# Kernel tuning notes

Hardware: AMD Instinct MI355X
Metric: run time of the kernel (lower is better)

The kernel has to match this reference:

```python
import jax, jax.numpy as jnp
import numpy as np

C = 256
GROUPS = 32
EPS = 1e-5

def setup_inputs() -> dict:
    key = jax.random.key(0)
    ks = jax.random.split(key, 7)
    B, H, W = 4, 64, 64
    x = jax.random.normal(ks[0], (B, C, H, W), dtype=jnp.float32)
    # GroupNorm affine params
    gn_w = jnp.ones((C,), dtype=jnp.float32)
    gn_b = jnp.zeros((C,), dtype=jnp.float32)
    # 1x1 conv weights stored as [out, in]
    s = 1.0 / np.sqrt(C)
    qkv_w = jax.random.uniform(ks[1], (3 * C, C), minval=-s, maxval=s, dtype=jnp.float32)
    qkv_b = jax.random.uniform(ks[2], (3 * C,), minval=-s, maxval=s, dtype=jnp.float32)
    proj_w = jax.random.uniform(ks[3], (C, C), minval=-s, maxval=s, dtype=jnp.float32)
    proj_b = jax.random.uniform(ks[4], (C,), minval=-s, maxval=s, dtype=jnp.float32)
    return {"x": x, "gn_w": gn_w, "gn_b": gn_b, "qkv_w": qkv_w,
            "qkv_b": qkv_b, "proj_w": proj_w, "proj_b": proj_b}

def group_norm(x, w, b):
    B, Cc, H, W = x.shape
    xg = x.reshape(B, GROUPS, Cc // GROUPS, H, W)
    mu = xg.mean(axis=(2, 3, 4), keepdims=True)
    var = xg.var(axis=(2, 3, 4), keepdims=True)
    xn = ((xg - mu) * jax.lax.rsqrt(var + EPS)).reshape(B, Cc, H, W)
    return xn * w[None, :, None, None] + b[None, :, None, None]

def reference(x, gn_w, gn_b, qkv_w, qkv_b, proj_w, proj_b):
    B, Cc, H, W = x.shape
    h = group_norm(x, gn_w, gn_b)
    # 1x1 conv == per-pixel matmul
    qkv = jnp.einsum('bchw,oc->bohw', h, qkv_w) + qkv_b[None, :, None, None]
    q, k, v = jnp.split(qkv, 3, axis=1)            # each [B, C, H, W]
    N = H * W
    q = q.reshape(B, Cc, N).transpose(0, 2, 1)      # [B, N, C]
    k = k.reshape(B, Cc, N)                         # [B, C, N]
    v = v.reshape(B, Cc, N).transpose(0, 2, 1)      # [B, N, C]
    w_att = jnp.einsum('bnc,bcm->bnm', q, k) * (Cc ** -0.5)
    w_att = jax.nn.softmax(w_att, axis=-1)
    h = jnp.einsum('bnm,bmc->bnc', w_att, v)        # [B, N, C]
    h = h.transpose(0, 2, 1).reshape(B, Cc, H, W)
    h = jnp.einsum('bchw,oc->bohw', h, proj_w) + proj_b[None, :, None, None]
    return x + h
```

## Files before the change

kernel.cpp:

```cpp
#include <hip/hip_runtime.h>
#include <stdint.h>

typedef unsigned short u16;
typedef __attribute__((ext_vector_type(8))) short bf16x8;
typedef __attribute__((ext_vector_type(4))) float f32x4;

#define BATCH   4
#define CH      256
#define NPIX    4096
#define NGROUPS 32
#define CPG     8
#define EPS     1e-5f

#define NSPLIT 4
#define SPLEN  (NPIX / NSPLIT)
#define ATK    32
#define NIT    (SPLEN / ATK)
#define WSTR   264
#define QTILES 2

__device__ __forceinline__ float bf2f(u16 u) {
    union { uint32_t i; float f; } v; v.i = ((uint32_t)u) << 16; return v.f;
}
__device__ __forceinline__ u16 f2bf(float f) {
    union { float f; uint32_t i; } v; v.f = f;
    uint32_t x = v.i;
    uint32_t r = (x + 0x7fffu + ((x >> 16) & 1u)) >> 16;
    return (u16)r;
}
__device__ __forceinline__ void unpack2(uint32_t u, float& a, float& b) {
    union { uint32_t i; float f; } lo, hi;
    lo.i = u << 16; hi.i = u & 0xffff0000u;
    a = lo.f; b = hi.f;
}
__device__ __forceinline__ void unpack8(uint4 u, float* f) {
    unpack2(u.x, f[0], f[1]); unpack2(u.y, f[2], f[3]);
    unpack2(u.z, f[4], f[5]); unpack2(u.w, f[6], f[7]);
}

__device__ __forceinline__ bool detect_f32(const void* xv) {
    const u16* p = (const u16*)xv;
    int bad = 0;
    #pragma unroll
    for (int i = 0; i < 32; i++) {
        u16 v = p[2 * i];
        int e = (v >> 7) & 0xff;
        bad += (e < 0x68 || e > 0x90) ? 1 : 0;
    }
    return bad >= 10;
}
__device__ __forceinline__ float load1(const void* b, size_t i, bool f32) {
    return f32 ? ((const float*)b)[i] : bf2f(((const u16*)b)[i]);
}
__device__ __forceinline__ void store1(void* b, size_t i, bool f32, float v) {
    if (f32) ((float*)b)[i] = v; else ((u16*)b)[i] = f2bf(v);
}
__device__ __forceinline__ void load4v(const void* base, size_t off, bool f32, float* f) {
    if (f32) {
        float4 a = *(const float4*)((const float*)base + off);
        f[0] = a.x; f[1] = a.y; f[2] = a.z; f[3] = a.w;
    } else {
        uint2 u = *(const uint2*)((const u16*)base + off);
        unpack2(u.x, f[0], f[1]); unpack2(u.y, f[2], f[3]);
    }
}
__device__ __forceinline__ void load8v(const void* base, size_t off, bool f32, float* f) {
    if (f32) {
        const float4* p = (const float4*)((const float*)base + off);
        float4 a = p[0], b = p[1];
        f[0] = a.x; f[1] = a.y; f[2] = a.z; f[3] = a.w;
        f[4] = b.x; f[5] = b.y; f[6] = b.z; f[7] = b.w;
    } else {
        uint4 u = *(const uint4*)((const u16*)base + off);
        unpack8(u, f);
    }
}

__global__ __launch_bounds__(256) void wconv(const void* __restrict__ qkv_w,
                                             const void* __restrict__ proj_w,
                                             u16* __restrict__ wq, u16* __restrict__ wp) {
    bool f32q = detect_f32(qkv_w);
    bool f32p = detect_f32(proj_w);
    int i = blockIdx.x * 256 + threadIdx.x;
    for (int e = i; e < 768 * 256; e += 256 * 256)
        wq[e] = f2bf(load1(qkv_w, e, f32q));
    for (int e = i; e < 256 * 256; e += 256 * 256)
        wp[e] = f2bf(load1(proj_w, e, f32p));
}

__global__ __launch_bounds__(256) void gn_stats(const void* __restrict__ x,
                                                float* __restrict__ stats, int b0) {
    bool f32 = detect_f32(x);
    int bg = b0 * NGROUPS + blockIdx.x;
    int t  = threadIdx.x;
    size_t base = (size_t)bg * (CPG * NPIX);
    float s = 0.f, s2 = 0.f;
    for (int i = t * 8; i < CPG * NPIX; i += 256 * 8) {
        float f[8]; load8v(x, base + i, f32, f);
        #pragma unroll
        for (int e = 0; e < 8; e++) { s += f[e]; s2 += f[e] * f[e]; }
    }
    #pragma unroll
    for (int off = 1; off < 64; off <<= 1) {
        s  += __shfl_xor(s,  off);
        s2 += __shfl_xor(s2, off);
    }
    __shared__ float red[8];
    int w = t >> 6;
    if ((t & 63) == 0) { red[w * 2] = s; red[w * 2 + 1] = s2; }
    __syncthreads();
    if (t == 0) {
        float S  = red[0] + red[2] + red[4] + red[6];
        float S2 = red[1] + red[3] + red[5] + red[7];
        float n  = (float)(CPG * NPIX);
        float mu = S / n;
        float var = S2 / n - mu * mu;
        stats[bg * 2]     = mu;
        stats[bg * 2 + 1] = rsqrtf(var + EPS);
    }
}

__global__ __launch_bounds__(256) void xgn(const void* __restrict__ x,
                                           const void* __restrict__ gn_w,
                                           const void* __restrict__ gn_b,
                                           const float* __restrict__ stats,
                                           u16* __restrict__ xt, int b0) {
    bool f32 = detect_f32(x);
    __shared__ u16 T[64][72];
    int bl = blockIdx.z, bg = b0 + bl;
    int n0 = blockIdx.x * 64, c0 = blockIdx.y * 64;
    int t = threadIdx.x;
    int tc = t >> 4, tn = (t & 15) * 4;
    #pragma unroll
    for (int i = 0; i < 4; i++) {
        int cl = tc + i * 16;
        int c = c0 + cl;
        int g = c >> 3;
        float mu = stats[(bg * NGROUPS + g) * 2];
        float rs = stats[(bg * NGROUPS + g) * 2 + 1];
        float wv = load1(gn_w, c, f32) * rs;
        float bv = load1(gn_b, c, f32) - mu * wv;
        float a[4];
        load4v(x, ((size_t)(bg * CH + c)) * NPIX + n0 + tn, f32, a);
        #pragma unroll
        for (int j = 0; j < 4; j++) T[cl][tn + j] = f2bf(a[j] * wv + bv);
    }
    __syncthreads();
    #pragma unroll
    for (int i = 0; i < 2; i++) {
        int e = t + i * 256;
        int nl = e >> 3, cc = (e & 7) * 8;
        union { uint4 v; u16 s[8]; } pk;
        #pragma unroll
        for (int j = 0; j < 8; j++) pk.s[j] = T[cc + j][nl];
        *(uint4*)(xt + ((size_t)(bl * NPIX) + n0 + nl) * CH + c0 + cc) = pk.v;
    }
}

__global__ __launch_bounds__(256, 3) void qkv_mfma(const u16* __restrict__ xt,
                                                   const u16* __restrict__ wq,
                                                   const void* __restrict__ qkv_b,
                                                   u16* __restrict__ qk,
                                                   u16* __restrict__ vt) {
    __shared__ u16 Ws[64 * WSTR];
    __shared__ u16 T2b[128 * 72];
    bool f32b = detect_f32(qkv_b);
    int bl = blockIdx.z;
    int o0 = blockIdx.y * 64;
    int t = threadIdx.x;
    int w = t >> 6, lane = t & 63;
    int l15 = lane & 15, quad = lane >> 4;

    #pragma unroll
    for (int i = 0; i < 8; i++) {
        int e = t + i * 256;
        *(uint4*)(Ws + (e >> 5) * WSTR + (e & 31) * 8) =
            *(const uint4*)(wq + (size_t)(o0 + (e >> 5)) * CH + (e & 31) * 8);
    }
    __syncthreads();

    bool isv = (o0 >= 512);
    for (int tt = 0; tt < QTILES; tt++) {
        int n0 = (blockIdx.x * QTILES + tt) * 128;
        int pbase = n0 + w * 32;
        const u16* xa = xt + ((size_t)(bl * NPIX + pbase)) * CH;

        f32x4 acc[2][4];
        #pragma unroll
        for (int m = 0; m < 2; m++)
            #pragma unroll
            for (int n = 0; n < 4; n++)
                #pragma unroll
                for (int r = 0; r < 4; r++) acc[m][n][r] = 0.f;

        #pragma unroll
        for (int kc = 0; kc < 8; kc++) {
            bf16x8 a0 = *(const bf16x8*)(xa + (size_t)(l15) * CH + kc * 32 + quad * 8);
            bf16x8 a1 = *(const bf16x8*)(xa + (size_t)(16 + l15) * CH + kc * 32 + quad * 8);
            #pragma unroll
            for (int n = 0; n < 4; n++) {
                bf16x8 b = *(const bf16x8*)(Ws + (n * 16 + l15) * WSTR + kc * 32 + quad * 8);
                acc[0][n] = __builtin_amdgcn_mfma_f32_16x16x32_bf16(a0, b, acc[0][n], 0, 0, 0);
                acc[1][n] = __builtin_amdgcn_mfma_f32_16x16x32_bf16(a1, b, acc[1][n], 0, 0, 0);
            }
        }

        if (!isv) {
            __syncthreads();
            #pragma unroll
            for (int n = 0; n < 4; n++) {
                int o = o0 + n * 16 + l15;
                float bias = load1(qkv_b, o, f32b);
                #pragma unroll
                for (int m = 0; m < 2; m++)
                    #pragma unroll
                    for (int r = 0; r < 4; r++) {
                        int prow = w * 32 + m * 16 + quad * 4 + r;
                        T2b[prow * 72 + n * 16 + l15] = f2bf(acc[m][n][r] + bias);
                    }
            }
            __syncthreads();
            #pragma unroll
            for (int i = 0; i < 4; i++) {
                int e = t + i * 256;
                int p = e >> 3, c = (e & 7) * 8;
                uint4 v = *(const uint4*)(T2b + p * 72 + c);
                *(uint4*)(qk + ((size_t)(bl * NPIX + n0 + p)) * 512 + o0 + c) = v;
            }
        } else {
            #pragma unroll
            for (int n = 0; n < 4; n++) {
                int o = o0 + n * 16 + l15;
                float bias = load1(qkv_b, o, f32b);
                size_t rowb = ((size_t)(bl * CH + o - 512)) * NPIX + pbase;
                #pragma unroll
                for (int m = 0; m < 2; m++) {
                    union { uint2 v; u16 s[4]; } pk;
                    #pragma unroll
                    for (int r = 0; r < 4; r++) pk.s[r] = f2bf(acc[m][n][r] + bias);
                    *(uint2*)(vt + rowb + quad * 8 + m * 4) = pk.v;
                }
            }
        }
    }
}

__global__ __launch_bounds__(256, 2) void attn_mfma(const u16* __restrict__ qk,
                                                    const u16* __restrict__ vt,
                                                    u16* __restrict__ Opart,
                                                    float* __restrict__ lpart,
                                                    int NE, int NR) {
    __shared__ u16 Ks[ATK * 256];
    __shared__ u16 Vts[CH * 32];
    int bl    = blockIdx.z;
    int split = blockIdx.y;
    int q0    = blockIdx.x * 128;
    int t     = threadIdx.x;
    int w     = t >> 6, lane = t & 63;
    int l15   = lane & 15, quad = lane >> 4;

    const u16* qkb = qk + (size_t)bl * NPIX * 512;
    const u16* vtb = vt + (size_t)bl * CH * NPIX;
    int kvbase = split * SPLEN;

    bf16x8 qf[2][8];
    #pragma unroll
    for (int m = 0; m < 2; m++) {
        const u16* qrow = qkb + (size_t)(q0 + w * 32 + m * 16 + l15) * 512;
        #pragma unroll
        for (int kc = 0; kc < 8; kc++)
            qf[m][kc] = *(const bf16x8*)(qrow + kc * 32 + quad * 8);
    }
    f32x4 o[2][16];
    #pragma unroll
    for (int m = 0; m < 2; m++)
        #pragma unroll
        for (int i = 0; i < 16; i++)
            #pragma unroll
            for (int r = 0; r < 4; r++) o[m][i][r] = 0.f;
    float lsum[2] = {0.f, 0.f};
    const float scale = 0.0625f;
    int swz = l15 & 7;

    for (int it = 0; it < NIT; it++) {
        int kv0 = kvbase + it * ATK;
        __syncthreads();
        #pragma unroll
        for (int i = 0; i < 4; i++) {
            int g = t + i * 256;
            int row = g >> 5, pcol = g & 31;
            int lcol = pcol ^ (row & 7);
            __builtin_amdgcn_global_load_lds(
                (const void*)(qkb + (size_t)(kv0 + row) * 512 + 256 + lcol * 8),
                (void*)(Ks + (size_t)g * 8), 16, 0, 0);
        }
        #pragma unroll
        for (int i = 0; i < 4; i++) {
            int g = t + i * 256;
            __builtin_amdgcn_global_load_lds(
                (const void*)(vtb + (size_t)(g >> 2) * NPIX + kv0 + (g & 3) * 8),
                (void*)(Vts + (size_t)g * 8), 16, 0, 0);
        }
        __syncthreads();

        f32x4 sT[2][2];
        #pragma unroll
        for (int kt = 0; kt < 2; kt++)
            #pragma unroll
            for (int qt = 0; qt < 2; qt++)
                #pragma unroll
                for (int r = 0; r < 4; r++) sT[kt][qt][r] = 0.f;
        #pragma unroll
        for (int kc = 0; kc < 8; kc++) {
            int sc = (kc * 4 + quad) ^ swz;
            bf16x8 a0 = *(const bf16x8*)(Ks + l15 * 256 + sc * 8);
            bf16x8 a1 = *(const bf16x8*)(Ks + (16 + l15) * 256 + sc * 8);
            sT[0][0] = __builtin_amdgcn_mfma_f32_16x16x32_bf16(a0, qf[0][kc], sT[0][0], 0, 0, 0);
            sT[0][1] = __builtin_amdgcn_mfma_f32_16x16x32_bf16(a0, qf[1][kc], sT[0][1], 0, 0, 0);
            sT[1][0] = __builtin_amdgcn_mfma_f32_16x16x32_bf16(a1, qf[0][kc], sT[1][0], 0, 0, 0);
            sT[1][1] = __builtin_amdgcn_mfma_f32_16x16x32_bf16(a1, qf[1][kc], sT[1][1], 0, 0, 0);
        }

        bf16x8 pa[2];
        #pragma unroll
        for (int qt = 0; qt < 2; qt++) {
            union { bf16x8 v; u16 s[8]; } pk;
            float ls = 0.f;
            #pragma unroll
            for (int kt = 0; kt < 2; kt++)
                #pragma unroll
                for (int r = 0; r < 4; r++) {
                    float p = __expf(sT[kt][qt][r] * scale);
                    ls += p;
                    pk.s[kt * 4 + r] = f2bf(p);
                }
            lsum[qt] += ls;
            pa[qt] = pk.v;
        }

        #pragma unroll
        for (int dt = 0; dt < 16; dt++) {
            bf16x8 vf = *(const bf16x8*)(Vts + (dt * 16 + l15) * 32 + quad * 8);
            o[0][dt] = __builtin_amdgcn_mfma_f32_16x16x32_bf16(pa[0], vf, o[0][dt], 0, 0, 0);
            o[1][dt] = __builtin_amdgcn_mfma_f32_16x16x32_bf16(pa[1], vf, o[1][dt], 0, 0, 0);
        }
    }

    size_t rowb = (size_t)bl * NPIX + q0 + w * 32;
    u16* op = Opart + (size_t)split * NE;
    #pragma unroll
    for (int qt = 0; qt < 2; qt++) {
        float v = lsum[qt];
        v += __shfl_xor(v, 16); v += __shfl_xor(v, 32);
        if (quad == 0)
            lpart[(size_t)split * NR + rowb + qt * 16 + l15] = v;
        #pragma unroll
        for (int dt = 0; dt < 16; dt++)
            #pragma unroll
            for (int r = 0; r < 4; r++)
                op[(rowb + qt * 16 + quad * 4 + r) * CH + dt * 16 + l15] = f2bf(o[qt][dt][r]);
    }
}

__global__ __launch_bounds__(256, 4) void proj_mfma(const u16* __restrict__ Opart,
                                                    const float* __restrict__ lpart,
                                                    const u16* __restrict__ wp,
                                                    const void* __restrict__ proj_b,
                                                    const void* __restrict__ x,
                                                    void* __restrict__ out,
                                                    int b0, int NE, int NR) {
    __shared__ u16 Ws[64 * WSTR];
    bool f32 = detect_f32(x);
    int bl = blockIdx.z, bg = b0 + bl;
    int n0 = blockIdx.x * 128, o0 = blockIdx.y * 64;
    int t = threadIdx.x;
    int w = t >> 6, lane = t & 63;
    int l15 = lane & 15, quad = lane >> 4;
    int pbase = n0 + w * 32;

    #pragma unroll
    for (int i = 0; i < 8; i++) {
        int e = t + i * 256;
        *(uint4*)(Ws + (e >> 5) * WSTR + (e & 31) * 8) =
            *(const uint4*)(wp + (size_t)(o0 + (e >> 5)) * CH + (e & 31) * 8);
    }
    __syncthreads();

    size_t rowg[2]; float invl[2];
    #pragma unroll
    for (int m = 0; m < 2; m++) {
        rowg[m] = (size_t)bl * NPIX + pbase + m * 16 + l15;
        float l = 0.f;
        #pragma unroll
        for (int s = 0; s < NSPLIT; s++) l += lpart[(size_t)s * NR + rowg[m]];
        invl[m] = 1.0f / l;
    }

    f32x4 acc[2][4];
    #pragma unroll
    for (int m = 0; m < 2; m++)
        #pragma unroll
        for (int n = 0; n < 4; n++)
            #pragma unroll
            for (int r = 0; r < 4; r++) acc[m][n][r] = 0.f;

    #pragma unroll
    for (int kc = 0; kc < 8; kc++) {
        bf16x8 afr[2];
        #pragma unroll
        for (int m = 0; m < 2; m++) {
            float f[8] = {0.f,0.f,0.f,0.f,0.f,0.f,0.f,0.f};
            #pragma unroll
            for (int s = 0; s < NSPLIT; s++) {
                bf16x8 v = *(const bf16x8*)(Opart + (size_t)s * NE + rowg[m] * CH + kc * 32 + quad * 8);
                #pragma unroll
                for (int j = 0; j < 8; j++) f[j] += bf2f((u16)v[j]);
            }
            bf16x8 a;
            #pragma unroll
            for (int j = 0; j < 8; j++) a[j] = (short)f2bf(f[j] * invl[m]);
            afr[m] = a;
        }
        #pragma unroll
        for (int n = 0; n < 4; n++) {
            bf16x8 b = *(const bf16x8*)(Ws + (n * 16 + l15) * WSTR + kc * 32 + quad * 8);
            acc[0][n] = __builtin_amdgcn_mfma_f32_16x16x32_bf16(afr[0], b, acc[0][n], 0, 0, 0);
            acc[1][n] = __builtin_amdgcn_mfma_f32_16x16x32_bf16(afr[1], b, acc[1][n], 0, 0, 0);
        }
    }

    __syncthreads();
    float4* T4 = (float4*)Ws;
    #pragma unroll
    for (int n = 0; n < 4; n++) {
        int o = o0 + n * 16 + l15;
        float bias = load1(proj_b, o, f32);
        #pragma unroll
        for (int m = 0; m < 2; m++) {
            float4 v;
            v.x = acc[m][n][0] + bias; v.y = acc[m][n][1] + bias;
            v.z = acc[m][n][2] + bias; v.w = acc[m][n][3] + bias;
            T4[(n * 16 + l15) * 33 + w * 8 + m * 4 + quad] = v;
        }
    }
    __syncthreads();
    const float* Tf = (const float*)Ws;
    if (f32) {
        #pragma unroll
        for (int i = 0; i < 8; i++) {
            int idx = t + i * 256;
            int row = idx >> 5, c4 = idx & 31;
            float4 v = T4[row * 33 + c4];
            size_t go = ((size_t)(bg * CH + o0 + row)) * NPIX + n0 + c4 * 4;
            float4 xr = *(const float4*)((const float*)x + go);
            v.x += xr.x; v.y += xr.y; v.z += xr.z; v.w += xr.w;
            *(float4*)((float*)out + go) = v;
        }
    } else {
        #pragma unroll
        for (int i = 0; i < 4; i++) {
            int idx = t + i * 256;
            int row = idx >> 4, c8 = idx & 15;
            size_t go = ((size_t)(bg * CH + o0 + row)) * NPIX + n0 + c8 * 8;
            uint4 xr = *(const uint4*)((const u16*)x + go);
            float xf[8]; unpack8(xr, xf);
            union { uint4 v; u16 s[8]; } pk;
            #pragma unroll
            for (int j = 0; j < 8; j++)
                pk.s[j] = f2bf(Tf[row * 132 + c8 * 8 + j] + xf[j]);
            *(uint4*)((u16*)out + go) = pk.v;
        }
    }
}

extern "C" void kernel_launch(void* const* d_in, const int* in_sizes, int n_in,
                              void* d_out, int out_size, void* d_ws, size_t ws_size,
                              hipStream_t stream) {
    const void* x      = d_in[0];
    const void* gn_w   = d_in[1];
    const void* gn_b   = d_in[2];
    const void* qkv_w  = d_in[3];
    const void* qkv_b  = d_in[4];
    const void* proj_w = d_in[5];
    const void* proj_b = d_in[6];

    char* ws = (char*)d_ws;
    float* stats = (float*)ws;
    u16* wq = (u16*)(ws + 1024);
    u16* wp = wq + 768 * 256;
    char* dyn = ws + 1024 + (768 * 256 + 256 * 256) * 2;

    const size_t per_batch = (size_t)NPIX * CH * 2
                           + (size_t)NPIX * 512 * 2
                           + (size_t)CH * NPIX * 2
                           + (size_t)NSPLIT * NPIX * CH * 2
                           + (size_t)NSPLIT * NPIX * 4;
    const size_t need_full = 1024 + 600 * 1024 + BATCH * per_batch;
    int nb = (ws_size >= need_full) ? BATCH : 1;

    u16* xt      = (u16*)dyn;
    u16* qk      = xt + (size_t)nb * NPIX * CH;
    u16* vt      = qk + (size_t)nb * NPIX * 512;
    u16* Opart   = vt + (size_t)nb * CH * NPIX;
    float* lpart = (float*)(Opart + (size_t)NSPLIT * nb * NPIX * CH);
    int NE = nb * NPIX * CH;
    int NR = nb * NPIX;

    wconv<<<dim3(256), 256, 0, stream>>>(qkv_w, proj_w, wq, wp);

    for (int b0 = 0; b0 < BATCH; b0 += nb) {
        gn_stats<<<dim3(nb * NGROUPS), 256, 0, stream>>>(x, stats, b0);
        xgn<<<dim3(NPIX / 64, CH / 64, nb), 256, 0, stream>>>(
            x, gn_w, gn_b, stats, xt, b0);
        qkv_mfma<<<dim3(NPIX / 128 / QTILES, 768 / 64, nb), 256, 0, stream>>>(
            xt, wq, qkv_b, qk, vt);
        attn_mfma<<<dim3(NPIX / 128, NSPLIT, nb), 256, 0, stream>>>(
            qk, vt, Opart, lpart, NE, NR);
        proj_mfma<<<dim3(NPIX / 128, CH / 64, nb), 256, 0, stream>>>(
            Opart, lpart, wp, proj_b, x, d_out, b0, NE, NR);
    }
}
```

Measured before the change: 208.9 us.

## Double-buffer K/V tiles in LDS and swizzle V tile layout

The attention kernel now keeps two LDS buffers for the K and V^T tiles. It prefetches the next tile with global_load_lds while the current tile is used for the QK and PV MFMAs, which leaves one barrier per iteration instead of two. This is meant to hide global-load latency behind compute. The V^T tile also gets an XOR swizzle on its 16-byte chunks to cut LDS bank conflicts on fragment reads. LDS use per block doubles, which could cap occupancy, and the compiler may still insert conservative waits on the async LDS loads.

```diff
diff --git a/kernel.cpp b/kernel.cpp
--- a/kernel.cpp
+++ b/kernel.cpp
@@ -250,8 +250,8 @@
                                                     u16* __restrict__ Opart,
                                                     float* __restrict__ lpart,
                                                     int NE, int NR) {
-    __shared__ u16 Ks[ATK * 256];
-    __shared__ u16 Vts[CH * 32];
+    __shared__ u16 Ks[2][ATK * 256];
+    __shared__ u16 Vts[2][CH * 32];
     int bl    = blockIdx.z;
     int split = blockIdx.y;
     int q0    = blockIdx.x * 128;
@@ -282,26 +282,51 @@
     const float scale = 0.0625f;
     int swz = l15 & 7;
 
+    #pragma unroll
+    for (int i = 0; i < 4; i++) {
+        int g = t + i * 256;
+        int row = g >> 5, pcol = g & 31;
+        int lcol = pcol ^ (row & 7);
+        __builtin_amdgcn_global_load_lds(
+            (const void*)(qkb + (size_t)(kvbase + row) * 512 + 256 + lcol * 8),
+            (void*)(&Ks[0][0] + (size_t)g * 8), 16, 0, 0);
+    }
+    #pragma unroll
+    for (int i = 0; i < 4; i++) {
+        int g = t + i * 256;
+        int row = g >> 2, s = g & 3;
+        __builtin_amdgcn_global_load_lds(
+            (const void*)(vtb + (size_t)row * NPIX + kvbase + (s ^ (row & 3)) * 8),
+            (void*)(&Vts[0][0] + (size_t)g * 8), 16, 0, 0);
+    }
+    __syncthreads();
+
     for (int it = 0; it < NIT; it++) {
-        int kv0 = kvbase + it * ATK;
-        __syncthreads();
-        #pragma unroll
-        for (int i = 0; i < 4; i++) {
-            int g = t + i * 256;
-            int row = g >> 5, pcol = g & 31;
-            int lcol = pcol ^ (row & 7);
-            __builtin_amdgcn_global_load_lds(
-                (const void*)(qkb + (size_t)(kv0 + row) * 512 + 256 + lcol * 8),
-                (void*)(Ks + (size_t)g * 8), 16, 0, 0);
-        }
-        #pragma unroll
-        for (int i = 0; i < 4; i++) {
-            int g = t + i * 256;
-            __builtin_amdgcn_global_load_lds(
-                (const void*)(vtb + (size_t)(g >> 2) * NPIX + kv0 + (g & 3) * 8),
-                (void*)(Vts + (size_t)g * 8), 16, 0, 0);
-        }
-        __syncthreads();
+        int cur = it & 1;
+        if (it + 1 < NIT) {
+            int kv1 = kvbase + (it + 1) * ATK;
+            u16* KsB = &Ks[cur ^ 1][0];
+            u16* VsB = &Vts[cur ^ 1][0];
+            #pragma unroll
+            for (int i = 0; i < 4; i++) {
+                int g = t + i * 256;
+                int row = g >> 5, pcol = g & 31;
+                int lcol = pcol ^ (row & 7);
+                __builtin_amdgcn_global_load_lds(
+                    (const void*)(qkb + (size_t)(kv1 + row) * 512 + 256 + lcol * 8),
+                    (void*)(KsB + (size_t)g * 8), 16, 0, 0);
+            }
+            #pragma unroll
+            for (int i = 0; i < 4; i++) {
+                int g = t + i * 256;
+                int row = g >> 2, s = g & 3;
+                __builtin_amdgcn_global_load_lds(
+                    (const void*)(vtb + (size_t)row * NPIX + kv1 + (s ^ (row & 3)) * 8),
+                    (void*)(VsB + (size_t)g * 8), 16, 0, 0);
+            }
+        }
+        const u16* KsC = &Ks[cur][0];
+        const u16* VsC = &Vts[cur][0];
 
         f32x4 sT[2][2];
         #pragma unroll
@@ -313,8 +338,8 @@
         #pragma unroll
         for (int kc = 0; kc < 8; kc++) {
             int sc = (kc * 4 + quad) ^ swz;
-            bf16x8 a0 = *(const bf16x8*)(Ks + l15 * 256 + sc * 8);
-            bf16x8 a1 = *(const bf16x8*)(Ks + (16 + l15) * 256 + sc * 8);
+            bf16x8 a0 = *(const bf16x8*)(KsC + l15 * 256 + sc * 8);
+            bf16x8 a1 = *(const bf16x8*)(KsC + (16 + l15) * 256 + sc * 8);
             sT[0][0] = __builtin_amdgcn_mfma_f32_16x16x32_bf16(a0, qf[0][kc], sT[0][0], 0, 0, 0);
             sT[0][1] = __builtin_amdgcn_mfma_f32_16x16x32_bf16(a0, qf[1][kc], sT[0][1], 0, 0, 0);
             sT[1][0] = __builtin_amdgcn_mfma_f32_16x16x32_bf16(a1, qf[0][kc], sT[1][0], 0, 0, 0);
@@ -340,10 +365,13 @@
 
         #pragma unroll
         for (int dt = 0; dt < 16; dt++) {
-            bf16x8 vf = *(const bf16x8*)(Vts + (dt * 16 + l15) * 32 + quad * 8);
+            int row = dt * 16 + l15;
+            bf16x8 vf = *(const bf16x8*)(VsC + row * 32 + (quad ^ (row & 3)) * 8);
             o[0][dt] = __builtin_amdgcn_mfma_f32_16x16x32_bf16(pa[0], vf, o[0][dt], 0, 0, 0);
             o[1][dt] = __builtin_amdgcn_mfma_f32_16x16x32_bf16(pa[1], vf, o[1][dt], 0, 0, 0);
         }
+
+        __syncthreads();
     }
 
     size_t rowb = (size_t)bl * NPIX + q0 + w * 32;
```

Result: no change. 208.8 us, median of 2 (-0.1%).
